# Optimization experiments

Measured on AMD Instinct MI355X. Metric: run time of the kernel, lower is better.

The kernel has to match this reference:

```python
import jax, jax.numpy as jnp
import numpy as np

B, C, H, W = 16, 512, 32, 32
NUM_HEADS = 8
GROUPS = 32
EPS = 1e-5


def setup_inputs() -> dict:
    key = jax.random.key(0)
    ks = jax.random.split(key, 3)
    x = jax.random.normal(ks[0], (B, C, H, W), dtype=jnp.float32)
    # Conv2d 1x1 weights stored as (out, in); init ~ fan-in scaled normal
    qkv_w = jax.random.normal(ks[1], (3 * C, C), dtype=jnp.float32) * (C ** -0.5)
    proj_w = jax.random.normal(ks[2], (C, C), dtype=jnp.float32) * (C ** -0.5)
    return {
        "x": x,
        "norm_w": jnp.ones((C,), jnp.float32),
        "norm_b": jnp.zeros((C,), jnp.float32),
        "qkv_w": qkv_w,
        "qkv_b": jnp.zeros((3 * C,), jnp.float32),
        "proj_w": proj_w,
        "proj_b": jnp.zeros((C,), jnp.float32),
    }


def reference(x, norm_w, norm_b, qkv_w, qkv_b, proj_w, proj_b):
    b, c, hh, ww = x.shape
    nh = NUM_HEADS
    hd = c // nh
    n = hh * ww

    # GroupNorm(32, C)
    xg = x.reshape(b, GROUPS, c // GROUPS, hh, ww)
    mean = xg.mean(axis=(2, 3, 4), keepdims=True)
    var = ((xg - mean) ** 2).mean(axis=(2, 3, 4), keepdims=True)
    hn = ((xg - mean) * jax.lax.rsqrt(var + EPS)).reshape(b, c, hh, ww)
    hn = hn * norm_w[None, :, None, None] + norm_b[None, :, None, None]

    # 1x1 conv QKV projection
    qkv = jnp.einsum('bchw,oc->bohw', hn, qkv_w) + qkv_b[None, :, None, None]
    # (B,3C,H,W) -> (B,3,nh,hd,N) -> (3,B,nh,N,hd)
    qkv = qkv.reshape(b, 3, nh, hd, n).transpose(1, 0, 2, 4, 3)
    q, k, v = qkv[0], qkv[1], qkv[2]

    scale = hd ** -0.5
    attn = jax.nn.softmax(jnp.einsum('bhnd,bhmd->bhnm', q, k) * scale, axis=-1)
    o = jnp.einsum('bhnm,bhmd->bhnd', attn, v)  # (B,nh,N,hd)
    o = o.transpose(0, 1, 3, 2).reshape(b, c, hh, ww)

    out = jnp.einsum('bchw,oc->bohw', o, proj_w) + proj_b[None, :, None, None]
    return out + x
```

## Files before the change

kernel.cpp:

```cpp
#include <hip/hip_runtime.h>
#include <cstdint>
#include <math.h>


typedef __bf16 bf16;
typedef __attribute__((ext_vector_type(8))) __bf16 bf16x8;
typedef __attribute__((ext_vector_type(4))) float f32x4;
typedef __attribute__((ext_vector_type(4))) short s16x4;

union U8 { uint4 u4; bf16x8 v; bf16 h[8]; };
union U4 { ushort4 u; bf16 h[4]; };
union UB4 { ushort4 u; s16x4 s; bf16 h[4]; };
union F4 { float4 v; float f[4]; };

typedef __attribute__((address_space(1))) void* gp1;
typedef __attribute__((address_space(3))) void* lp3;

__device__ __forceinline__ void async16(const void* g, void* l) {
  __builtin_amdgcn_global_load_lds((gp1)g, (lp3)l, 16, 0, 0);
}

#define LOG2E 1.44269504f

__global__ __launch_bounds__(256) void cvt_w(const float* __restrict__ qw,
                                             const float* __restrict__ pw,
                                             bf16* __restrict__ qwb,
                                             bf16* __restrict__ pwb) {
  int i = blockIdx.x * 256 + threadIdx.x;
  F4 v; bf16* dst;
  if (i < 196608) { v.v = ((const float4*)qw)[i]; dst = qwb + (size_t)i * 4; }
  else { v.v = ((const float4*)pw)[i - 196608]; dst = pwb + (size_t)(i - 196608) * 4; }
  U4 o;
#pragma unroll
  for (int j = 0; j < 4; j++) o.h[j] = (bf16)v.f[j];
  *(ushort4*)dst = o.u;
}

__global__ __launch_bounds__(256) void gn_stats(const float* __restrict__ x,
                                                float2* __restrict__ stats) {
  int bg = blockIdx.x;
  const float* base = x + (size_t)bg * 16384;
  int t = threadIdx.x;
  float s = 0.f, ss = 0.f;
#pragma unroll
  for (int p = 0; p < 16; p++) {
    F4 u; u.v = *(const float4*)(base + (size_t)(p * 256 + t) * 4);
#pragma unroll
    for (int i = 0; i < 4; i++) { float v = u.f[i]; s += v; ss += v * v; }
  }
  for (int off = 1; off < 64; off <<= 1) { s += __shfl_xor(s, off); ss += __shfl_xor(ss, off); }
  __shared__ float red[8];
  int w = t >> 6;
  if ((t & 63) == 0) { red[w] = s; red[4 + w] = ss; }
  __syncthreads();
  if (t == 0) {
    float S = red[0] + red[1] + red[2] + red[3];
    float SS = red[4] + red[5] + red[6] + red[7];
    float mean = S * (1.f / 16384.f);
    float var = SS * (1.f / 16384.f) - mean * mean;
    stats[bg] = make_float2(mean, rsqrtf(var + 1e-5f));
  }
}

__global__ __launch_bounds__(256) void gn_apply(const float* __restrict__ x,
                                                const float* __restrict__ nwp,
                                                const float* __restrict__ nbp,
                                                const float2* __restrict__ stats,
                                                bf16* __restrict__ hnt) {
  int b = blockIdx.z, nt = blockIdx.y, ct = blockIdx.x;
  int t = threadIdx.x, w = t >> 6, l = t & 63;
  int wc = w & 1, wn = w >> 1;
  int cb = ct * 128 + wc * 64 + (l & 7) * 8;
  int n0 = nt * 64 + wn * 32 + (l >> 3) * 4;
  float2 ms = stats[b * 32 + (cb >> 4)];
  float wgt[8], bia[8];
#pragma unroll
  for (int i = 0; i < 8; i++) {
    float wi = nwp[cb + i] * ms.y;
    wgt[i] = wi;
    bia[i] = nbp[cb + i] - ms.x * wi;
  }
  F4 in[8];
  const float* xb = x + ((size_t)b * 512 + cb) * 1024 + n0;
#pragma unroll
  for (int i = 0; i < 8; i++) in[i].v = *(const float4*)(xb + (size_t)i * 1024);
  bf16* ob = hnt + ((size_t)b * 1024 + n0) * 512 + cb;
#pragma unroll
  for (int j = 0; j < 4; j++) {
    U8 o;
#pragma unroll
    for (int i = 0; i < 8; i++) o.h[i] = (bf16)(in[i].f[j] * wgt[i] + bia[i]);
    *(uint4*)(ob + (size_t)j * 512) = o.u4;
  }
}

__device__ __forceinline__ void gemm_bt_core(const bf16* ga0, const bf16* gb0,
                                             bf16* At, bf16* Bt,
                                             f32x4 (&acc)[4][4], int w, int l) {
  const bf16* ga = ga0 + (size_t)(w * 16 + (l >> 2)) * 512 + (l & 3) * 8;
  const bf16* gb = gb0 + (size_t)(w * 16 + (l >> 2)) * 512 + (l & 3) * 8;
  int wr = w >> 1, wc = w & 1;
  const bf16* Ab = At + (wr * 64 + (l & 15)) * 32 + (l >> 4) * 8;
  const bf16* Bb = Bt + (wc * 64 + (l & 15)) * 32 + (l >> 4) * 8;
  bf16* lA = At + w * 16 * 32;
  bf16* lB = Bt + w * 16 * 32;
  for (int k0 = 0; k0 < 512; k0 += 32) {
    async16(ga + k0, lA);
    async16(ga + 64 * 512 + k0, lA + 64 * 32);
    async16(gb + k0, lB);
    async16(gb + 64 * 512 + k0, lB + 64 * 32);
    __syncthreads();
    bf16x8 af[4], bfr[4];
#pragma unroll
    for (int i = 0; i < 4; i++) {
      af[i] = *(const bf16x8*)(Ab + i * 512);
      bfr[i] = *(const bf16x8*)(Bb + i * 512);
    }
#pragma unroll
    for (int i = 0; i < 4; i++)
#pragma unroll
      for (int j = 0; j < 4; j++)
        acc[i][j] = __builtin_amdgcn_mfma_f32_16x16x32_bf16(af[i], bfr[j], acc[i][j], 0, 0, 0);
    __syncthreads();
  }
}

__global__ __launch_bounds__(256, 2) void qkv_gemm(const bf16* __restrict__ hnt,
                                                   const bf16* __restrict__ qwb,
                                                   const float* __restrict__ qb,
                                                   bf16* __restrict__ qsw,
                                                   bf16* __restrict__ ksw,
                                                   bf16* __restrict__ vsw) {
  __shared__ bf16 At[128 * 32];
  __shared__ bf16 Bt[128 * 32];
  int b = blockIdx.z, mt = blockIdx.y, ot = blockIdx.x;
  int m0 = mt * 128, o0 = ot * 128;
  int t = threadIdx.x, w = t >> 6, l = t & 63;
  f32x4 acc[4][4] = {};
  gemm_bt_core(hnt + ((size_t)b * 1024 + m0) * 512, qwb + (size_t)o0 * 512, At, Bt, acc, w, l);

  int wr = w >> 1, wc = w & 1, quad = l >> 4, li = l & 15;
#pragma unroll
  for (int i = 0; i < 4; i++) {
    int gnb = m0 + wr * 64 + i * 16;
    int blk = gnb >> 4;
#pragma unroll
    for (int j = 0; j < 4; j++) {
      int go = o0 + wc * 64 + j * 16 + li;
      float bias = qb[go];
      if (ot < 8) {
        int c = (ot < 4) ? go : (go - 512);
        int hh = c >> 6, d = c & 63;
        int ks = d >> 5, dq = (d >> 3) & 3, jj = d & 7;
        bf16* base = ((ot < 4) ? qsw : ksw) + ((size_t)(b * 8 + hh) << 16)
                     + (blk * 2 + ks) * 512 + dq * 8 + jj;
#pragma unroll
        for (int r = 0; r < 4; r++)
          base[(quad * 4 + r) * 32] = (bf16)(acc[i][j][r] + bias);
      } else {
        int c = go - 1024;
        int hh = c >> 6, d = c & 63;
        int df = d >> 4, lv = d & 15;
        bf16* base = vsw + ((size_t)(b * 8 + hh) << 16)
                     + (blk * 4 + df) * 256 + (lv * 4 + quad) * 4;
        U4 pk;
#pragma unroll
        for (int r = 0; r < 4; r++) pk.h[r] = (bf16)(acc[i][j][r] + bias);
        *(ushort4*)base = pk.u;
      }
    }
  }
}

__device__ __forceinline__ void attn_stage(const bf16* __restrict__ kp,
                                           const bf16* __restrict__ vp, int c,
                                           f32x4 (&stc)[2][2],
                                           f32x4 (&stn)[2][2],
                                           U8 (&ka)[2], U8 (&kc)[2],
                                           const bf16x8 (&qfr)[2][2],
                                           float (&mrun)[2], f32x4 (&lacc)[2],
                                           f32x4 (&of)[4][2]) {
#pragma unroll
  for (int qf = 0; qf < 2; qf++)
#pragma unroll
    for (int kf = 0; kf < 2; kf++) stn[qf][kf] = (f32x4){0.f, 0.f, 0.f, 0.f};
  __builtin_amdgcn_s_setprio(1);
#pragma unroll
  for (int kf = 0; kf < 2; kf++) {
    stn[0][kf] = __builtin_amdgcn_mfma_f32_16x16x32_bf16(ka[kf].v, qfr[0][0], stn[0][kf], 0, 0, 0);
    stn[1][kf] = __builtin_amdgcn_mfma_f32_16x16x32_bf16(ka[kf].v, qfr[1][0], stn[1][kf], 0, 0, 0);
    stn[0][kf] = __builtin_amdgcn_mfma_f32_16x16x32_bf16(kc[kf].v, qfr[0][1], stn[0][kf], 0, 0, 0);
    stn[1][kf] = __builtin_amdgcn_mfma_f32_16x16x32_bf16(kc[kf].v, qfr[1][1], stn[1][kf], 0, 0, 0);
  }
  __builtin_amdgcn_s_setprio(0);
  int cb = c * 2048;
  UB4 va[2][4];
#pragma unroll
  for (int kf = 0; kf < 2; kf++)
#pragma unroll
    for (int df = 0; df < 4; df++)
      va[kf][df].u = *(const ushort4*)(vp + cb + kf * 1024 + df * 256);
  int cn = ((c + 2) & 31) * 2048;
#pragma unroll
  for (int kf = 0; kf < 2; kf++) {
    ka[kf].u4 = *(const uint4*)(kp + cn + kf * 1024);
    kc[kf].u4 = *(const uint4*)(kp + cn + kf * 1024 + 512);
  }
  UB4 pfr[2][2];
#pragma unroll
  for (int qf = 0; qf < 2; qf++) {
    float mt = fmaxf(fmaxf(fmaxf(stc[qf][0][0], stc[qf][0][1]),
                           fmaxf(stc[qf][0][2], stc[qf][0][3])),
                     fmaxf(fmaxf(stc[qf][1][0], stc[qf][1][1]),
                           fmaxf(stc[qf][1][2], stc[qf][1][3])));
    if (__ballot(mt > mrun[qf] + 8.f)) {
      mt = fmaxf(mt, __shfl_xor(mt, 16));
      mt = fmaxf(mt, __shfl_xor(mt, 32));
      float mnew = fmaxf(mrun[qf], mt);
      float alpha = __builtin_amdgcn_exp2f(mrun[qf] - mnew);
      mrun[qf] = mnew;
#pragma unroll
      for (int r = 0; r < 4; r++) lacc[qf][r] *= alpha;
#pragma unroll
      for (int df = 0; df < 4; df++)
#pragma unroll
        for (int r = 0; r < 4; r++) of[df][qf][r] *= alpha;
    }
    float m = mrun[qf];
#pragma unroll
    for (int kf = 0; kf < 2; kf++)
#pragma unroll
      for (int r = 0; r < 4; r++) {
        float e = __builtin_amdgcn_exp2f(stc[qf][kf][r] - m);
        lacc[qf][r] += e;
        pfr[qf][kf].h[r] = (bf16)e;
      }
  }
  __builtin_amdgcn_s_setprio(1);
#pragma unroll
  for (int kf = 0; kf < 2; kf++)
#pragma unroll
    for (int df = 0; df < 4; df++)
#pragma unroll
      for (int qf = 0; qf < 2; qf++)
        of[df][qf] = __builtin_amdgcn_mfma_f32_16x16x16bf16_1k(va[kf][df].s, pfr[qf][kf].s, of[df][qf], 0, 0, 0);
  __builtin_amdgcn_s_setprio(0);
}

__global__ __launch_bounds__(256, 3) void attn(const bf16* __restrict__ qsw,
                                               const bf16* __restrict__ ksw,
                                               const bf16* __restrict__ vsw,
                                               bf16* __restrict__ ont) {
  int bh = blockIdx.x;
  int b = bh >> 3, h = bh & 7;
  int qt = blockIdx.y;
  int t = threadIdx.x, w = t >> 6, l = t & 63;
  int quad = l >> 4, li = l & 15;
  int q0 = qt * 128 + w * 32;

  int laneK = (li * 4 + quad) * 8;
  int laneV = (li * 4 + quad) * 4;
  const bf16* qp = qsw + ((size_t)bh << 16) + laneK;
  const bf16* kp = ksw + ((size_t)bh << 16) + laneK;
  const bf16* vp = vsw + ((size_t)bh << 16) + laneV;

  const float QS = 0.125f * LOG2E;
  bf16x8 qfr[2][2];
#pragma unroll
  for (int qf = 0; qf < 2; qf++)
#pragma unroll
    for (int ks = 0; ks < 2; ks++) {
      U8 u;
      u.u4 = *(const uint4*)(qp + (((q0 >> 4) + qf) * 2 + ks) * 512);
#pragma unroll
      for (int i = 0; i < 8; i++) u.h[i] = (bf16)((float)u.h[i] * QS);
      qfr[qf][ks] = u.v;
    }

  float mrun[2] = {-INFINITY, -INFINITY};
  f32x4 lacc[2] = {};
  f32x4 of[4][2] = {};

  U8 ka[2], kc[2];
#pragma unroll
  for (int kf = 0; kf < 2; kf++) {
    ka[kf].u4 = *(const uint4*)(kp + kf * 1024);
    kc[kf].u4 = *(const uint4*)(kp + kf * 1024 + 512);
  }
  f32x4 st0[2][2] = {}, st1[2][2];
  __builtin_amdgcn_s_setprio(1);
#pragma unroll
  for (int kf = 0; kf < 2; kf++) {
    st0[0][kf] = __builtin_amdgcn_mfma_f32_16x16x32_bf16(ka[kf].v, qfr[0][0], st0[0][kf], 0, 0, 0);
    st0[1][kf] = __builtin_amdgcn_mfma_f32_16x16x32_bf16(ka[kf].v, qfr[1][0], st0[1][kf], 0, 0, 0);
    st0[0][kf] = __builtin_amdgcn_mfma_f32_16x16x32_bf16(kc[kf].v, qfr[0][1], st0[0][kf], 0, 0, 0);
    st0[1][kf] = __builtin_amdgcn_mfma_f32_16x16x32_bf16(kc[kf].v, qfr[1][1], st0[1][kf], 0, 0, 0);
  }
  __builtin_amdgcn_s_setprio(0);
#pragma unroll
  for (int kf = 0; kf < 2; kf++) {
    ka[kf].u4 = *(const uint4*)(kp + 2048 + kf * 1024);
    kc[kf].u4 = *(const uint4*)(kp + 2048 + kf * 1024 + 512);
  }

  for (int c = 0; c < 32; c += 2) {
    attn_stage(kp, vp, c,     st0, st1, ka, kc, qfr, mrun, lacc, of);
    attn_stage(kp, vp, c + 1, st1, st0, ka, kc, qfr, mrun, lacc, of);
  }

#pragma unroll
  for (int qf = 0; qf < 2; qf++) {
    float lsum = (lacc[qf][0] + lacc[qf][1]) + (lacc[qf][2] + lacc[qf][3]);
    lsum += __shfl_xor(lsum, 16);
    lsum += __shfl_xor(lsum, 32);
    float inv = 1.f / lsum;
    bf16* ob = ont + ((size_t)b * 1024 + q0 + qf * 16 + li) * 512 + h * 64 + quad * 4;
#pragma unroll
    for (int df = 0; df < 4; df++) {
      U4 pk;
#pragma unroll
      for (int r = 0; r < 4; r++) pk.h[r] = (bf16)(of[df][qf][r] * inv);
      *(ushort4*)(ob + df * 16) = pk.u;
    }
  }
}

__global__ __launch_bounds__(256, 2) void proj_gemm(const bf16* __restrict__ ont,
                                                    const bf16* __restrict__ pwb,
                                                    const float* __restrict__ pb,
                                                    const float* __restrict__ x,
                                                    float* __restrict__ out) {
  __shared__ bf16 At[128 * 32];
  __shared__ bf16 Bt[128 * 32];
  int b = blockIdx.z, mt = blockIdx.y, ot = blockIdx.x;
  int m0 = mt * 128, o0 = ot * 128;
  int t = threadIdx.x, w = t >> 6, l = t & 63;
  f32x4 acc[4][4] = {};
  gemm_bt_core(ont + ((size_t)b * 1024 + m0) * 512, pwb + (size_t)o0 * 512, At, Bt, acc, w, l);

  int wr = w >> 1, wc = w & 1, quad = l >> 4, li = l & 15;
#pragma unroll
  for (int i = 0; i < 4; i++) {
    int gn = m0 + wr * 64 + i * 16 + quad * 4;
#pragma unroll
    for (int j = 0; j < 4; j++) {
      int go = o0 + wc * 64 + j * 16 + li;
      float bias = pb[go];
      F4 xres; xres.v = *(const float4*)(x + ((size_t)b * 512 + go) * 1024 + gn);
      F4 o;
#pragma unroll
      for (int r = 0; r < 4; r++) o.f[r] = acc[i][j][r] + bias + xres.f[r];
      *(float4*)(out + ((size_t)b * 512 + go) * 1024 + gn) = o.v;
    }
  }
}

extern "C" void kernel_launch(void* const* d_in, const int* in_sizes, int n_in,
                              void* d_out, int out_size, void* d_ws, size_t ws_size,
                              hipStream_t stream) {
  const float* x  = (const float*)d_in[0];
  const float* nw = (const float*)d_in[1];
  const float* nb = (const float*)d_in[2];
  const float* qw = (const float*)d_in[3];
  const float* qb = (const float*)d_in[4];
  const float* pw = (const float*)d_in[5];
  const float* pb = (const float*)d_in[6];
  float* out = (float*)d_out;

  char* ws = (char*)d_ws;
  float2* stats = (float2*)ws;
  bf16* qwb = (bf16*)(ws + (64u << 10));
  bf16* pwb = (bf16*)(ws + (2u << 20));
  bf16* hnt = (bf16*)(ws + (4u << 20));
  bf16* qsw = (bf16*)(ws + (20u << 20));
  bf16* ksw = (bf16*)(ws + (36u << 20));
  bf16* vsw = (bf16*)(ws + (52u << 20));
  bf16* ont = hnt;

  cvt_w<<<1024, 256, 0, stream>>>(qw, pw, qwb, pwb);
  gn_stats<<<512, 256, 0, stream>>>(x, stats);
  gn_apply<<<dim3(4, 16, 16), 256, 0, stream>>>(x, nw, nb, stats, hnt);
  qkv_gemm<<<dim3(12, 8, 16), 256, 0, stream>>>(hnt, qwb, qb, qsw, ksw, vsw);
  attn<<<dim3(128, 8, 1), 256, 0, stream>>>(qsw, ksw, vsw, ont);
  proj_gemm<<<dim3(4, 8, 16), 256, 0, stream>>>(ont, pwb, pb, x, out);
}
```

Before: 231.6 us.

## Double-buffer LDS tiles in GEMM core to overlap loads with MFMA

```diff
diff --git a/kernel.cpp b/kernel.cpp
--- a/kernel.cpp
+++ b/kernel.cpp
@@ -94,50 +94,71 @@
   }
 }
 
+__device__ __forceinline__ void gemm_compute32(const bf16* __restrict__ rA,
+                                               const bf16* __restrict__ rB,
+                                               int aoff, int boff,
+                                               f32x4 (&acc)[4][4]) {
+  bf16x8 af[4], bfr[4];
+#pragma unroll
+  for (int i = 0; i < 4; i++) {
+    af[i] = *(const bf16x8*)(rA + aoff + i * 512);
+    bfr[i] = *(const bf16x8*)(rB + boff + i * 512);
+  }
+#pragma unroll
+  for (int i = 0; i < 4; i++)
+#pragma unroll
+    for (int j = 0; j < 4; j++)
+      acc[i][j] = __builtin_amdgcn_mfma_f32_16x16x32_bf16(af[i], bfr[j], acc[i][j], 0, 0, 0);
+}
+
 __device__ __forceinline__ void gemm_bt_core(const bf16* ga0, const bf16* gb0,
-                                             bf16* At, bf16* Bt,
+                                             bf16* A0, bf16* B0,
+                                             bf16* A1, bf16* B1,
                                              f32x4 (&acc)[4][4], int w, int l) {
   const bf16* ga = ga0 + (size_t)(w * 16 + (l >> 2)) * 512 + (l & 3) * 8;
   const bf16* gb = gb0 + (size_t)(w * 16 + (l >> 2)) * 512 + (l & 3) * 8;
   int wr = w >> 1, wc = w & 1;
-  const bf16* Ab = At + (wr * 64 + (l & 15)) * 32 + (l >> 4) * 8;
-  const bf16* Bb = Bt + (wc * 64 + (l & 15)) * 32 + (l >> 4) * 8;
-  bf16* lA = At + w * 16 * 32;
-  bf16* lB = Bt + w * 16 * 32;
-  for (int k0 = 0; k0 < 512; k0 += 32) {
-    async16(ga + k0, lA);
-    async16(ga + 64 * 512 + k0, lA + 64 * 32);
-    async16(gb + k0, lB);
-    async16(gb + 64 * 512 + k0, lB + 64 * 32);
+  int aoff = (wr * 64 + (l & 15)) * 32 + (l >> 4) * 8;
+  int boff = (wc * 64 + (l & 15)) * 32 + (l >> 4) * 8;
+  int soff = w * 16 * 32;
+
+  async16(ga, A0 + soff);
+  async16(ga + 64 * 512, A0 + soff + 64 * 32);
+  async16(gb, B0 + soff);
+  async16(gb + 64 * 512, B0 + soff + 64 * 32);
+  __syncthreads();
+
+  for (int k0 = 0; k0 < 512; k0 += 64) {
+    async16(ga + k0 + 32, A1 + soff);
+    async16(ga + 64 * 512 + k0 + 32, A1 + soff + 64 * 32);
+    async16(gb + k0 + 32, B1 + soff);
+    async16(gb + 64 * 512 + k0 + 32, B1 + soff + 64 * 32);
+    gemm_compute32(A0, B0, aoff, boff, acc);
     __syncthreads();
-    bf16x8 af[4], bfr[4];
-#pragma unroll
-    for (int i = 0; i < 4; i++) {
-      af[i] = *(const bf16x8*)(Ab + i * 512);
-      bfr[i] = *(const bf16x8*)(Bb + i * 512);
-    }
-#pragma unroll
-    for (int i = 0; i < 4; i++)
-#pragma unroll
-      for (int j = 0; j < 4; j++)
-        acc[i][j] = __builtin_amdgcn_mfma_f32_16x16x32_bf16(af[i], bfr[j], acc[i][j], 0, 0, 0);
+    if (k0 + 64 < 512) {
+      async16(ga + k0 + 64, A0 + soff);
+      async16(ga + 64 * 512 + k0 + 64, A0 + soff + 64 * 32);
+      async16(gb + k0 + 64, B0 + soff);
+      async16(gb + 64 * 512 + k0 + 64, B0 + soff + 64 * 32);
+    }
+    gemm_compute32(A1, B1, aoff, boff, acc);
     __syncthreads();
   }
 }
 
-__global__ __launch_bounds__(256, 2) void qkv_gemm(const bf16* __restrict__ hnt,
+__global__ __launch_bounds__(256, 3) void qkv_gemm(const bf16* __restrict__ hnt,
                                                    const bf16* __restrict__ qwb,
                                                    const float* __restrict__ qb,
                                                    bf16* __restrict__ qsw,
                                                    bf16* __restrict__ ksw,
                                                    bf16* __restrict__ vsw) {
-  __shared__ bf16 At[128 * 32];
-  __shared__ bf16 Bt[128 * 32];
+  __shared__ bf16 A0[128 * 32], B0[128 * 32], A1[128 * 32], B1[128 * 32];
   int b = blockIdx.z, mt = blockIdx.y, ot = blockIdx.x;
   int m0 = mt * 128, o0 = ot * 128;
   int t = threadIdx.x, w = t >> 6, l = t & 63;
   f32x4 acc[4][4] = {};
-  gemm_bt_core(hnt + ((size_t)b * 1024 + m0) * 512, qwb + (size_t)o0 * 512, At, Bt, acc, w, l);
+  gemm_bt_core(hnt + ((size_t)b * 1024 + m0) * 512, qwb + (size_t)o0 * 512,
+               A0, B0, A1, B1, acc, w, l);
 
   int wr = w >> 1, wc = w & 1, quad = l >> 4, li = l & 15;
 #pragma unroll
@@ -325,18 +346,18 @@
   }
 }
 
-__global__ __launch_bounds__(256, 2) void proj_gemm(const bf16* __restrict__ ont,
+__global__ __launch_bounds__(256, 3) void proj_gemm(const bf16* __restrict__ ont,
                                                     const bf16* __restrict__ pwb,
                                                     const float* __restrict__ pb,
                                                     const float* __restrict__ x,
                                                     float* __restrict__ out) {
-  __shared__ bf16 At[128 * 32];
-  __shared__ bf16 Bt[128 * 32];
+  __shared__ bf16 A0[128 * 32], B0[128 * 32], A1[128 * 32], B1[128 * 32];
   int b = blockIdx.z, mt = blockIdx.y, ot = blockIdx.x;
   int m0 = mt * 128, o0 = ot * 128;
   int t = threadIdx.x, w = t >> 6, l = t & 63;
   f32x4 acc[4][4] = {};
-  gemm_bt_core(ont + ((size_t)b * 1024 + m0) * 512, pwb + (size_t)o0 * 512, At, Bt, acc, w, l);
+  gemm_bt_core(ont + ((size_t)b * 1024 + m0) * 512, pwb + (size_t)o0 * 512,
+               A0, B0, A1, B1, acc, w, l);
 
   int wr = w >> 1, wc = w & 1, quad = l >> 4, li = l & 15;
 #pragma unroll
```

Result: no change. 230.1 us (-0.7%).
